# Performance work log

Hardware: AMD Instinct MI355X
Metric: run time of the kernel (lower is better)

## Reference

```python
import jax, jax.numpy as jnp
import numpy as np

K = 9        # kNN neighbors (ViG default kernel_size=9)
EPS = 1e-5   # BatchNorm eps


def _bn2d(x, gamma, beta):
    # training-mode BatchNorm2d over (B,H,W) per channel; x: [B,C,H,W]
    mean = jnp.mean(x, axis=(0, 2, 3), keepdims=True)
    var = jnp.var(x, axis=(0, 2, 3), keepdims=True)
    g = gamma.reshape(1, -1, 1, 1)
    b = beta.reshape(1, -1, 1, 1)
    return g * (x - mean) * jax.lax.rsqrt(var + EPS) + b


def setup_inputs() -> dict:
    key = jax.random.key(0)
    B, C, H, W = 8, 96, 56, 56
    oup = 192
    ks = jax.random.split(key, 8)
    sc = 0.05
    return {
        "x": jax.random.normal(ks[0], (B, C, H, W), dtype=jnp.float32),
        "W_fc1": jax.random.normal(ks[1], (C, C), dtype=jnp.float32) * sc,
        "b_fc1": jnp.zeros((C,), jnp.float32),
        "g_bn1": jnp.ones((C,), jnp.float32),
        "be_bn1": jnp.zeros((C,), jnp.float32),
        "W_edge": jax.random.normal(ks[2], (2 * C, 2 * C), dtype=jnp.float32) * sc,
        "b_edge": jnp.zeros((2 * C,), jnp.float32),
        "g_bne": jnp.ones((2 * C,), jnp.float32),
        "be_bne": jnp.zeros((2 * C,), jnp.float32),
        "W_fc2": jax.random.normal(ks[3], (2 * C, C), dtype=jnp.float32) * sc,
        "b_fc2": jnp.zeros((C,), jnp.float32),
        "g_bn2": jnp.ones((C,), jnp.float32),
        "be_bn2": jnp.zeros((C,), jnp.float32),
        "g_sabn": jnp.ones((C,), jnp.float32),
        "be_sabn": jnp.zeros((C,), jnp.float32),
        "W_dw": jax.random.normal(ks[4], (oup, C, 3, 3), dtype=jnp.float32) * sc,
        "b_dw": jnp.zeros((oup,), jnp.float32),
        "g_dwbn": jnp.ones((oup,), jnp.float32),
        "be_dwbn": jnp.zeros((oup,), jnp.float32),
    }


def reference(x, W_fc1, b_fc1, g_bn1, be_bn1, W_edge, b_edge, g_bne, be_bne,
              W_fc2, b_fc2, g_bn2, be_bn2, g_sabn, be_sabn,
              W_dw, b_dw, g_dwbn, be_dwbn):
    B, C, H, W = x.shape
    N = H * W
    shortcut = x

    # --- Grapher.fc1: 1x1 conv + BN ---
    y = jnp.einsum('bchw,cd->bdhw', x, W_fc1) + b_fc1[None, :, None, None]
    y = _bn2d(y, g_bn1, be_bn1)

    # --- dynamic kNN graph over flattened tokens ---
    ft = y.reshape(B, C, N).transpose(0, 2, 1)            # [B,N,C]
    sq = jnp.sum(ft * ft, axis=-1)                        # [B,N]
    dist = sq[:, :, None] - 2.0 * jnp.einsum('bnc,bmc->bnm', ft, ft) + sq[:, None, :]
    _, idx = jax.lax.top_k(-dist, K)                      # [B,N,K] nearest neighbors

    # --- EdgeConv: max_k act(BN(W [x_i, x_j - x_i])) ---
    x_j = jnp.take_along_axis(ft[:, :, None, :], idx[..., None], axis=1)  # [B,N,K,C]
    x_i = ft[:, :, None, :]                               # [B,N,1,C]
    e = jnp.concatenate([jnp.broadcast_to(x_i, x_j.shape), x_j - x_i], axis=-1)  # [B,N,K,2C]
    e = jnp.einsum('bnkc,cd->bnkd', e, W_edge) + b_edge
    m = jnp.mean(e, axis=(0, 1, 2))
    v = jnp.var(e, axis=(0, 1, 2))
    e = g_bne * (e - m) * jax.lax.rsqrt(v + EPS) + be_bne
    e = jax.nn.relu(e)
    g = jnp.max(e, axis=2)                                # [B,N,2C] max-aggregation

    # --- Grapher.fc2: 1x1 conv + BN, residual ---
    g = jnp.einsum('bnc,cd->bnd', g, W_fc2) + b_fc2       # [B,N,C]
    g = g.transpose(0, 2, 1).reshape(B, C, H, W)
    g = _bn2d(g, g_bn2, be_bn2)
    y = g + shortcut

    # --- SAEncoder: BN + ReLU ---
    y = jax.nn.relu(_bn2d(y, g_sabn, be_sabn))

    # --- convdw: 3x3 stride-2 conv + BN + ReLU ---
    y = jax.lax.conv_general_dilated(
        y, W_dw, window_strides=(2, 2), padding=((1, 1), (1, 1)),
        dimension_numbers=('NCHW', 'OIHW', 'NCHW')) + b_dw[None, :, None, None]
    y = jax.nn.relu(_bn2d(y, g_dwbn, be_dwbn))
    return y
```

## Files before the change

kernel.cpp:

```cpp
#include <hip/hip_runtime.h>
#include <math.h>

#define B_   8
#define C_   96
#define C2_  192
#define N_   3136
#define R_   25088
#define OUP_ 192
#define HO_  28
#define NO_  784
#define EPS_ 1e-5f
#define QS2  128
#define CAP3 64

typedef short bf16x8 __attribute__((ext_vector_type(8)));
typedef float f32x4  __attribute__((ext_vector_type(4)));

__device__ __forceinline__ int swz16(int i) { return (i & ~15) | ((i & 15) ^ ((i >> 4) & 7)); }

__global__ __launch_bounds__(512) void k_fc1_d(const float* __restrict__ x,
                                               const float* __restrict__ W1,
                                               const float* __restrict__ b1,
                                               double* __restrict__ yd) {
    __shared__ double Wl[96 * 48];
    int tid = threadIdx.x;
    int rl = tid & 255, h = tid >> 8;
    int dbase = blockIdx.y * 48;
    for (int q = tid; q < 96 * 48; q += 512) {
        int c = q / 48, dd = q % 48;
        Wl[c * 48 + dd] = (double)W1[c * 96 + dbase + dd];
    }
    __syncthreads();
    int r = blockIdx.x * 256 + rl;
    int b = r / N_;
    int n = r - b * N_;
    double acc[24];
#pragma unroll
    for (int i = 0; i < 24; i++) acc[i] = 0.0;
    const float* xp = x + (size_t)b * C_ * N_ + n;
    for (int c = 0; c < 96; ++c) {
        double xv = (double)xp[(size_t)c * N_];
        const double* w = &Wl[c * 48 + h * 24];
#pragma unroll
        for (int i = 0; i < 24; ++i) acc[i] += xv * w[i];
    }
    int d0 = dbase + h * 24;
#pragma unroll
    for (int i = 0; i < 24; i++) {
        int d = d0 + i;
        yd[((size_t)b * C_ + d) * N_ + n] = acc[i] + (double)b1[d];
    }
}

__global__ __launch_bounds__(256) void k_stats_chan_d(const double* __restrict__ src,
                                                      double* __restrict__ partial) {
    int c = blockIdx.x;
    int chunk = blockIdx.y;
    const int SPLIT = 16;
    double s = 0.0, ss = 0.0;
    for (int j = chunk * 256 + threadIdx.x; j < R_; j += SPLIT * 256) {
        int b = j / N_, n = j - b * N_;
        double v = src[((size_t)b * C_ + c) * N_ + n];
        s += v;
        ss += v * v;
    }
    __shared__ double red[8];
    for (int off = 32; off; off >>= 1) {
        s += __shfl_down(s, off, 64);
        ss += __shfl_down(ss, off, 64);
    }
    int lane = threadIdx.x & 63, w = threadIdx.x >> 6;
    if (lane == 0) { red[w * 2] = s; red[w * 2 + 1] = ss; }
    __syncthreads();
    if (threadIdx.x == 0) {
        s = red[0] + red[2] + red[4] + red[6];
        ss = red[1] + red[3] + red[5] + red[7];
        partial[(c * SPLIT + chunk) * 2] = s;
        partial[(c * SPLIT + chunk) * 2 + 1] = ss;
    }
}

__global__ void k_stats_reduce_d(const double* __restrict__ partial, double* __restrict__ stats) {
    int c = blockIdx.x * blockDim.x + threadIdx.x;
    if (c >= 96) return;
    double s = 0.0, ss = 0.0;
    for (int k = 0; k < 16; k++) {
        s += partial[(c * 16 + k) * 2];
        ss += partial[(c * 16 + k) * 2 + 1];
    }
    double m = s / (double)R_;
    double var = ss / (double)R_ - m * m;
    stats[c * 2] = m;
    stats[c * 2 + 1] = 1.0 / sqrt(var + 1e-5);
}

__global__ void k_stats_reduce(const float* __restrict__ partial, float* __restrict__ stats,
                               int Cn, int SPLIT, float invcount) {
    int c = blockIdx.x * blockDim.x + threadIdx.x;
    if (c >= Cn) return;
    float s = 0.f, ss = 0.f;
    for (int k = 0; k < SPLIT; k++) {
        s += partial[(c * SPLIT + k) * 2];
        ss += partial[(c * SPLIT + k) * 2 + 1];
    }
    float m = s * invcount;
    float var = ss * invcount - m * m;
    stats[c * 2] = m;
    stats[c * 2 + 1] = 1.0f / sqrtf(var + EPS_);
}

__global__ __launch_bounds__(256) void k_stats_reduce_g(const float* __restrict__ partial,
                                                        float* __restrict__ stats,
                                                        int Cn, int NB, float invcount) {
    int c = blockIdx.x;
    float s = 0.f, ss = 0.f;
    for (int k = threadIdx.x; k < NB; k += 256) {
        s  += partial[(size_t)k * 2 * Cn + c];
        ss += partial[(size_t)k * 2 * Cn + Cn + c];
    }
    __shared__ float red[8];
    for (int off = 32; off; off >>= 1) {
        s += __shfl_down(s, off, 64);
        ss += __shfl_down(ss, off, 64);
    }
    int lane = threadIdx.x & 63, w = threadIdx.x >> 6;
    if (lane == 0) { red[w * 2] = s; red[w * 2 + 1] = ss; }
    __syncthreads();
    if (threadIdx.x == 0) {
        s = red[0] + red[2] + red[4] + red[6];
        ss = red[1] + red[3] + red[5] + red[7];
        float m = s * invcount;
        float var = ss * invcount - m * m;
        stats[c * 2] = m;
        stats[c * 2 + 1] = 1.0f / sqrtf(var + EPS_);
    }
}

__global__ __launch_bounds__(256) void k_bn1_tr(const double* __restrict__ yd,
                                                const double* __restrict__ stats,
                                                const float* __restrict__ g,
                                                const float* __restrict__ be,
                                                float* __restrict__ ftc,
                                                double* __restrict__ ftp64,
                                                unsigned short* __restrict__ fspH,
                                                double* __restrict__ sq64,
                                                unsigned* __restrict__ poolCnt) {
    __shared__ double tile[64 * 97];
    __shared__ double dsq[64][4];
    int b = blockIdx.y;
    int n0 = blockIdx.x * 64;
    int tid = threadIdx.x;
    int n = tid & 63, w = tid >> 6;
    for (int k = 0; k < 24; ++k) {
        int c = k * 4 + w;
        size_t gi = ((size_t)b * C_ + c) * N_ + n0 + n;
        double m = stats[c * 2], rs = stats[c * 2 + 1];
        double v = (double)g[c] * (yd[gi] - m) * rs + (double)be[c];
        ftc[gi] = (float)v;
        tile[n * 97 + c] = v;
    }
    __syncthreads();
    int p = n, q = w;
    double vals[24];
    double s = 0.0;
    const double* lp = &tile[p * 97 + q * 24];
#pragma unroll
    for (int m2 = 0; m2 < 24; ++m2) { vals[m2] = lp[m2]; s += vals[m2] * vals[m2]; }
    dsq[p][q] = s;
    double* dst = ftp64 + ((size_t)b * N_ + n0 + p) * C_ + q * 24;
#pragma unroll
    for (int m2 = 0; m2 < 24; m2 += 2) *(double2*)&dst[m2] = make_double2(vals[m2], vals[m2 + 1]);
    unsigned* hdst = (unsigned*)(fspH + ((size_t)b * N_ + n0 + p) * QS2);
#pragma unroll
    for (int m2 = 0; m2 < 24; m2 += 2) {
        unsigned u0 = __float_as_uint((float)vals[m2]);
        unsigned u1 = __float_as_uint((float)vals[m2 + 1]);
        unsigned h0 = (u0 + 0x7fffu + ((u0 >> 16) & 1u)) >> 16;
        unsigned h1 = (u1 + 0x7fffu + ((u1 >> 16) & 1u)) >> 16;
        hdst[q * 12 + (m2 >> 1)] = h0 | (h1 << 16);
    }
    __syncthreads();
    if (tid < 64) {
        double tot = dsq[tid][0] + dsq[tid][1] + dsq[tid][2] + dsq[tid][3];
        sq64[(size_t)b * N_ + n0 + tid] = tot;
        poolCnt[(size_t)b * N_ + n0 + tid] = 0u;
        float t32 = (float)(-0.5 * tot);
        unsigned u0 = __float_as_uint(t32);
        unsigned h0 = (u0 + 0x7fffu + ((u0 >> 16) & 1u)) >> 16;
        float resid = t32 - __uint_as_float(h0 << 16);
        unsigned u1 = __float_as_uint(resid);
        unsigned h1 = (u1 + 0x7fffu + ((u1 >> 16) & 1u)) >> 16;
        unsigned* hd = (unsigned*)(fspH + ((size_t)b * N_ + n0 + tid) * QS2);
        hd[48] = h0 | (h1 << 16);
#pragma unroll
        for (int k2 = 49; k2 < 64; ++k2) hd[k2] = 0u;
    }
}

__global__ __launch_bounds__(256) void k_dist5(const unsigned short* __restrict__ fspH,
                                               unsigned short* __restrict__ poolC,
                                               unsigned* __restrict__ poolCnt) {
    __shared__ __align__(16) char lds[39680];
    float* cminF = (float*)(lds + 32768);
    float* t9fL  = (float*)(lds + 39168);
    int b = blockIdx.z, half = blockIdx.y;
    int q0 = blockIdx.x * 64;
    int tid = threadIdx.x, w = tid >> 6, l = tid & 63;
    int ch0 = half * 25, nch = half ? 24 : 25;
    int qg = b * N_ + q0 + w * 16 + (l & 15);

    {
        const uint4* src = (const uint4*)(fspH + ((size_t)b * N_ + q0) * QS2);
        uint4* dst = (uint4*)lds;
        for (int i = tid; i < 1024; i += 256) dst[swz16(i)] = src[i];
    }
    __syncthreads();
    bf16x8 Bq[4];
    {
        const unsigned short* Ql = (const unsigned short*)lds;
        int qr = w * 16 + (l & 15);
#pragma unroll
        for (int s = 0; s < 3; ++s) {
            int col = (s * 4 + (l >> 4)) ^ (qr & 7);
            Bq[s] = *(const bf16x8*)&Ql[qr * QS2 + col * 8];
        }
        bf16x8 z = {0, 0, 0, 0, 0, 0, 0, 0};
        if ((l >> 4) == 0) { z[0] = (short)0x3F80; z[1] = (short)0x3F80; }
        Bq[3] = z;
    }
    __syncthreads();

    {
        const uint4* src = (const uint4*)(fspH + ((size_t)b * N_ + ch0 * 64) * QS2);
        uint4* dst = (uint4*)lds;
        for (int i = tid; i < 1024; i += 256) dst[swz16(i)] = src[i];
    }
    __syncthreads();

    float thr2r = 1e30f;
    int cur = 0;
    int nct = 2 * nch;
    for (int t = 0; t < nct; ++t) {
        int chl = (t < nch) ? t : t - nch;
        int c0 = (ch0 + chl) * 64;
        bool pf = (t < nct - 1);
        uint4 st0, st1, st2, st3;
        if (pf) {
            int tn = t + 1;
            int nc = ch0 + ((tn < nch) ? tn : tn - nch);
            const uint4* src = (const uint4*)(fspH + ((size_t)b * N_ + nc * 64) * QS2);
            st0 = src[tid]; st1 = src[tid + 256]; st2 = src[tid + 512]; st3 = src[tid + 768];
        }
        const unsigned short* Bc = (const unsigned short*)(lds + cur * 16384);
        f32x4 acc[4];
#pragma unroll
        for (int ct = 0; ct < 4; ++ct) acc[ct] = (f32x4){0.f, 0.f, 0.f, 0.f};
#pragma unroll
        for (int s = 0; s < 4; ++s) {
#pragma unroll
            for (int ct = 0; ct < 4; ++ct) {
                int cr = ct * 16 + (l & 15);
                int col = (s * 4 + (l >> 4)) ^ (cr & 7);
                bf16x8 Ac = *(const bf16x8*)&Bc[cr * QS2 + col * 8];
                acc[ct] = __builtin_amdgcn_mfma_f32_16x16x32_bf16(Ac, Bq[s], acc[ct], 0, 0, 0);
            }
        }
        if (t < nch) {
            float mx = -1e30f;
#pragma unroll
            for (int ct = 0; ct < 4; ++ct)
#pragma unroll
                for (int j = 0; j < 4; ++j) mx = fmaxf(mx, acc[ct][j]);
            mx = fmaxf(mx, __shfl_xor(mx, 16, 64));
            mx = fmaxf(mx, __shfl_xor(mx, 32, 64));
            if (l < 16) cminF[chl * 64 + w * 16 + l] = -2.f * mx;
        } else {
#pragma unroll
            for (int ct = 0; ct < 4; ++ct)
#pragma unroll
                for (int j = 0; j < 4; ++j) {
                    if (acc[ct][j] >= thr2r) {
                        unsigned pos = atomicAdd(&poolCnt[qg], 1u);
                        if (pos < (unsigned)CAP3)
                            poolC[(size_t)qg * CAP3 + pos] = (unsigned short)(c0 + ct * 16 + (l >> 4) * 4 + j);
                    }
                }
        }
        if (t == nch - 1) {
            __syncthreads();
            if (tid < 64) {
                float top[9];
#pragma unroll
                for (int j = 0; j < 9; ++j) top[j] = 1e30f;
                for (int q = 0; q < nch; ++q) {
                    float v = cminF[q * 64 + tid];
                    if (v < top[8]) {
                        top[8] = v;
#pragma unroll
                        for (int j = 8; j >= 1; --j)
                            if (top[j] < top[j - 1]) { float tt = top[j]; top[j] = top[j - 1]; top[j - 1] = tt; }
                    }
                }
                float t9 = top[8] + fabsf(top[8]) * 0.008f + 0.75f;
                t9fL[tid] = -0.5f * t9;
            }
            __syncthreads();
            thr2r = t9fL[w * 16 + (l & 15)];
        }
        if (pf) {
            uint4* dst = (uint4*)(lds + (cur ^ 1) * 16384);
            dst[swz16(tid)] = st0;
            dst[swz16(tid + 256)] = st1;
            dst[swz16(tid + 512)] = st2;
            dst[swz16(tid + 768)] = st3;
        }
        __syncthreads();
        cur ^= 1;
    }
}

__global__ __launch_bounds__(256) void k_rerank_d(const unsigned short* __restrict__ poolC,
                                                  const unsigned* __restrict__ poolCnt,
                                                  const double* __restrict__ ftp64,
                                                  const double* __restrict__ sq64,
                                                  int* __restrict__ idx) {
    int tid = threadIdx.x;
    int wv = tid >> 6, l = tid & 63;
    int rr = blockIdx.x * 4 + wv;
    int b = rr / N_;
    int cnt = (int)poolCnt[rr];
    if (cnt > CAP3) cnt = CAP3;
    int e = l & 3;
    double qreg[24];
    {
        const double* qb = ftp64 + (size_t)rr * C_ + e * 24;
#pragma unroll
        for (int m = 0; m < 24; ++m) qreg[m] = qb[m];
    }
    double dv[4];
    int jv[4];
#pragma unroll
    for (int gG = 0; gG < 4; ++gG) { dv[gG] = 1e300; jv[gG] = 0x7fffffff; }
#pragma unroll
    for (int gG = 0; gG < 4; ++gG) {
        if (gG * 16 >= cnt) break;
        int ci = gG * 16 + (l >> 2);
        bool valid = ci < cnt;
        int j = valid ? (int)poolC[(size_t)rr * CAP3 + ci] : 0;
        const double* cb = ftp64 + ((size_t)b * N_ + j) * C_ + e * 24;
        double p = 0.0;
#pragma unroll
        for (int m = 0; m < 24; ++m) p += qreg[m] * cb[m];
        p += __shfl_xor(p, 1, 64);
        p += __shfl_xor(p, 2, 64);
        if (valid) {
            dv[gG] = sq64[(size_t)b * N_ + j] - 2.0 * p;
            jv[gG] = j;
        }
    }
#pragma unroll
    for (int r = 0; r < 9; ++r) {
        double dm = dv[0]; int jm = jv[0];
#pragma unroll
        for (int gG = 1; gG < 4; ++gG)
            if (dv[gG] < dm || (dv[gG] == dm && jv[gG] < jm)) { dm = dv[gG]; jm = jv[gG]; }
#pragma unroll
        for (int off = 1; off <= 32; off <<= 1) {
            double od = __shfl_xor(dm, off, 64);
            int oj = __shfl_xor(jm, off, 64);
            if (od < dm || (od == dm && oj < jm)) { dm = od; jm = oj; }
        }
        if (l == 0) idx[(size_t)rr * 9 + r] = jm;
#pragma unroll
        for (int gG = 0; gG < 4; ++gG)
            if (jv[gG] == jm) dv[gG] = 1e300;
    }
}

__global__ __launch_bounds__(512) void k_gemm_uv2(const float* __restrict__ ftc,
                                                  const float* __restrict__ We,
                                                  const float* __restrict__ beb,
                                                  float* __restrict__ u,
                                                  float* __restrict__ v) {
    __shared__ float Wl[2][96 * 48];
    int tid = threadIdx.x;
    int rl = tid & 255, h = tid >> 8;
    int dbase = blockIdx.y * 48;
    for (int q = tid; q < 96 * 48; q += 512) {
        int c = q / 48, dd = q % 48;
        float wb = We[(96 + c) * C2_ + dbase + dd];
        Wl[1][q] = wb;
        Wl[0][q] = We[c * C2_ + dbase + dd] - wb;
    }
    __syncthreads();
    int r = blockIdx.x * 256 + rl;
    int b = r / N_, n = r - b * N_;
    float a0[24], a1[24];
#pragma unroll
    for (int i = 0; i < 24; i++) { a0[i] = 0.f; a1[i] = 0.f; }
    const float* xp = ftc + (size_t)b * C_ * N_ + n;
    for (int c = 0; c < 96; ++c) {
        float xv = xp[(size_t)c * N_];
        const float4* w40 = (const float4*)&Wl[0][c * 48 + h * 24];
        const float4* w41 = (const float4*)&Wl[1][c * 48 + h * 24];
#pragma unroll
        for (int i = 0; i < 6; ++i) {
            float4 w0 = w40[i], w1 = w41[i];
            a0[i * 4 + 0] += xv * w0.x; a0[i * 4 + 1] += xv * w0.y;
            a0[i * 4 + 2] += xv * w0.z; a0[i * 4 + 3] += xv * w0.w;
            a1[i * 4 + 0] += xv * w1.x; a1[i * 4 + 1] += xv * w1.y;
            a1[i * 4 + 2] += xv * w1.z; a1[i * 4 + 3] += xv * w1.w;
        }
    }
    int d0 = dbase + h * 24;
    float* up = u + (size_t)r * C2_ + d0;
    float* vp = v + (size_t)r * C2_ + d0;
#pragma unroll
    for (int i = 0; i < 6; ++i) {
        float4 ou, ov;
        ou.x = a0[i * 4 + 0] + beb[d0 + i * 4 + 0];
        ou.y = a0[i * 4 + 1] + beb[d0 + i * 4 + 1];
        ou.z = a0[i * 4 + 2] + beb[d0 + i * 4 + 2];
        ou.w = a0[i * 4 + 3] + beb[d0 + i * 4 + 3];
        ov.x = a1[i * 4 + 0]; ov.y = a1[i * 4 + 1];
        ov.z = a1[i * 4 + 2]; ov.w = a1[i * 4 + 3];
        ((float4*)up)[i] = ou;
        ((float4*)vp)[i] = ov;
    }
}

__global__ __launch_bounds__(192) void k_bne_stats(const float* __restrict__ u,
                                                   const float* __restrict__ v,
                                                   const int* __restrict__ idx,
                                                   float* __restrict__ partial) {
    int d = threadIdx.x;
    int row0 = blockIdx.x * 32;
    int b = row0 / N_;
    float s = 0.f, ss = 0.f;
    for (int r = 0; r < 32; ++r) {
        int row = row0 + r;
        float ud = u[(size_t)row * C2_ + d];
        const int* ip = idx + (size_t)row * 9;
#pragma unroll
        for (int k = 0; k < 9; k++) {
            int j = ip[k];
            float e = ud + v[((size_t)b * N_ + j) * C2_ + d];
            s += e;
            ss += e * e;
        }
    }
    partial[(size_t)blockIdx.x * 384 + d] = s;
    partial[(size_t)blockIdx.x * 384 + 192 + d] = ss;
}

__global__ __launch_bounds__(192) void k_edge_fc2_st(const float* __restrict__ u,
                                                     const float* __restrict__ v,
                                                     const int* __restrict__ idx,
                                                     const float* __restrict__ statsE,
                                                     const float* __restrict__ ge,
                                                     const float* __restrict__ bee,
                                                     const float* __restrict__ W2,
                                                     const float* __restrict__ b2,
                                                     float* __restrict__ out2,
                                                     float* __restrict__ partialE) {
    __shared__ float gl[16][C2_];
    __shared__ float g2[C_][16];
    int tid = threadIdx.x;
    int row0 = blockIdx.x * 16;
    int b = row0 / N_;
    int n0 = row0 - b * N_;
    {
        int d = tid;
        float m = statsE[d * 2], rs = statsE[d * 2 + 1];
        float ga = ge[d], bb = bee[d];
        for (int r = 0; r < 16; ++r) {
            int row = row0 + r;
            float ud = u[(size_t)row * C2_ + d];
            const int* ip = idx + (size_t)row * 9;
            float gm = 0.f;
#pragma unroll
            for (int k = 0; k < 9; k++) {
                int j = ip[k];
                float e = ud + v[((size_t)b * N_ + j) * C2_ + d];
                float val = ga * (e - m) * rs + bb;
                gm = fmaxf(gm, val);
            }
            gl[r][d] = gm;
        }
    }
    __syncthreads();
    {
        int rr = tid / 24;
        int dq = tid % 24;
        for (int rep = 0; rep < 2; ++rep) {
            int r = rr + rep * 8;
            float4 acc = *(const float4*)&b2[dq * 4];
            for (int d = 0; d < C2_; ++d) {
                float gv = gl[r][d];
                float4 w = *(const float4*)&W2[d * C_ + dq * 4];
                acc.x += gv * w.x;
                acc.y += gv * w.y;
                acc.z += gv * w.z;
                acc.w += gv * w.w;
            }
            g2[dq * 4 + 0][r] = acc.x;
            g2[dq * 4 + 1][r] = acc.y;
            g2[dq * 4 + 2][r] = acc.z;
            g2[dq * 4 + 3][r] = acc.w;
        }
    }
    __syncthreads();
    for (int q = tid; q < 96 * 4; q += 192) {
        int dd = q / 4, part = q % 4;
        float4 val = *(const float4*)&g2[dd][part * 4];
        *(float4*)&out2[((size_t)b * C_ + dd) * N_ + n0 + part * 4] = val;
    }
    {
        int c = tid >> 1, h = tid & 1;
        float s = 0.f, ss = 0.f;
#pragma unroll
        for (int r = 0; r < 8; ++r) {
            float vv = g2[c][h * 8 + r];
            s += vv;
            ss += vv * vv;
        }
        s += __shfl_xor(s, 1, 64);
        ss += __shfl_xor(ss, 1, 64);
        if (h == 0) {
            partialE[(size_t)blockIdx.x * 192 + c] = s;
            partialE[(size_t)blockIdx.x * 192 + 96 + c] = ss;
        }
    }
}

__global__ __launch_bounds__(256) void k_bn2_add_st(const float* __restrict__ out2,
                                                    const float* __restrict__ x,
                                                    const float* __restrict__ stats,
                                                    const float* __restrict__ g,
                                                    const float* __restrict__ be,
                                                    float* __restrict__ t,
                                                    float* __restrict__ partial) {
    int c = blockIdx.x;
    int chunk = blockIdx.y;
    const int SPLIT = 16;
    float m = stats[c * 2], rs = stats[c * 2 + 1];
    float ga = g[c], bb = be[c];
    float s = 0.f, ss = 0.f;
    for (int j = chunk * 256 + threadIdx.x; j < R_; j += SPLIT * 256) {
        int b = j / N_, n = j - b * N_;
        size_t i = ((size_t)b * C_ + c) * N_ + n;
        float tv = ga * (out2[i] - m) * rs + bb + x[i];
        t[i] = tv;
        s += tv;
        ss += tv * tv;
    }
    __shared__ float red[8];
    for (int off = 32; off; off >>= 1) {
        s += __shfl_down(s, off, 64);
        ss += __shfl_down(ss, off, 64);
    }
    int lane = threadIdx.x & 63, w = threadIdx.x >> 6;
    if (lane == 0) { red[w * 2] = s; red[w * 2 + 1] = ss; }
    __syncthreads();
    if (threadIdx.x == 0) {
        s = red[0] + red[2] + red[4] + red[6];
        ss = red[1] + red[3] + red[5] + red[7];
        partial[(c * SPLIT + chunk) * 2] = s;
        partial[(c * SPLIT + chunk) * 2 + 1] = ss;
    }
}

__global__ __launch_bounds__(256) void k_conv8(const float* __restrict__ t,
                                               const float* __restrict__ statsS,
                                               const float* __restrict__ gS,
                                               const float* __restrict__ beS,
                                               const float* __restrict__ Wd,
                                               const float* __restrict__ bd,
                                               float* __restrict__ z,
                                               float* __restrict__ partialD) {
    __shared__ float Wl[96 * 9 * 8];
    __shared__ float scl[96], shf[96];
    __shared__ float redc[4][16];
    int b = blockIdx.z;
    int oc0 = blockIdx.y * 8;
    int p = blockIdx.x * 256 + threadIdx.x;
    for (int i = threadIdx.x; i < 96 * 9 * 8; i += 256) {
        int oc = i & 7, icq = i >> 3;
        Wl[i] = Wd[(size_t)(oc0 + oc) * 864 + icq];
    }
    if (threadIdx.x < 96) {
        int c = threadIdx.x;
        float m = statsS[c * 2], rs = statsS[c * 2 + 1], ga = gS[c];
        scl[c] = ga * rs;
        shf[c] = beS[c] - ga * m * rs;
    }
    __syncthreads();
    bool valid = p < NO_;
    int oh = valid ? p / HO_ : 0, ow = valid ? p % HO_ : 0;
    float acc[8];
#pragma unroll
    for (int i = 0; i < 8; i++) acc[i] = 0.f;
    int ih0 = oh * 2 - 1, iw0 = ow * 2 - 1;
    const float* tb = t + (size_t)b * C_ * N_;
    for (int ic = 0; ic < 96; ++ic) {
        const float* sp = tb + (size_t)ic * N_;
        float sc_ = scl[ic], sh_ = shf[ic];
        float in[9];
#pragma unroll
        for (int kh = 0; kh < 3; kh++) {
            int ih = ih0 + kh;
            bool okh = valid && ((unsigned)ih < 56u);
#pragma unroll
            for (int kw = 0; kw < 3; kw++) {
                int iw = iw0 + kw;
                bool ok = okh && ((unsigned)iw < 56u);
                float raw = ok ? sp[ih * 56 + iw] : 0.f;
                in[kh * 3 + kw] = ok ? fmaxf(sc_ * raw + sh_, 0.f) : 0.f;
            }
        }
#pragma unroll
        for (int q = 0; q < 9; q++) {
            float iv = in[q];
            const float4* w4 = (const float4*)&Wl[(ic * 9 + q) * 8];
#pragma unroll
            for (int j = 0; j < 2; j++) {
                float4 w = w4[j];
                acc[j * 4 + 0] += iv * w.x;
                acc[j * 4 + 1] += iv * w.y;
                acc[j * 4 + 2] += iv * w.z;
                acc[j * 4 + 3] += iv * w.w;
            }
        }
    }
    float s8[8];
#pragma unroll
    for (int i = 0; i < 8; i++) {
        float ov = acc[i] + bd[oc0 + i];
        if (valid) z[((size_t)b * OUP_ + oc0 + i) * NO_ + p] = ov;
        s8[i] = valid ? ov : 0.f;
    }
    int w = threadIdx.x >> 6;
#pragma unroll
    for (int i = 0; i < 8; ++i) {
        float s = s8[i], ss = s8[i] * s8[i];
        for (int off = 32; off; off >>= 1) {
            s += __shfl_down(s, off, 64);
            ss += __shfl_down(ss, off, 64);
        }
        if ((threadIdx.x & 63) == 0) { redc[w][i * 2] = s; redc[w][i * 2 + 1] = ss; }
    }
    __syncthreads();
    if (threadIdx.x < 16) {
        float v = redc[0][threadIdx.x] + redc[1][threadIdx.x] + redc[2][threadIdx.x] + redc[3][threadIdx.x];
        int blk = (b * 24 + blockIdx.y) * 4 + blockIdx.x;
        partialD[blk * 16 + threadIdx.x] = v;
    }
}

__global__ void k_stats_reduce_conv(const float* __restrict__ partialD, float* __restrict__ stats) {
    int c = threadIdx.x;
    if (c >= 192) return;
    int y = c >> 3, o = c & 7;
    float s = 0.f, ss = 0.f;
    for (int bb = 0; bb < 8; ++bb)
        for (int x2 = 0; x2 < 4; ++x2) {
            int blk = (bb * 24 + y) * 4 + x2;
            s += partialD[blk * 16 + o * 2];
            ss += partialD[blk * 16 + o * 2 + 1];
        }
    float m = s / 6272.f;
    float var = ss / 6272.f - m * m;
    stats[c * 2] = m;
    stats[c * 2 + 1] = 1.0f / sqrtf(var + EPS_);
}

__global__ __launch_bounds__(256) void k_out(const float* __restrict__ z,
                                             const float* __restrict__ stats,
                                             const float* __restrict__ g,
                                             const float* __restrict__ be,
                                             float* __restrict__ out) {
    int i = blockIdx.x * 256 + threadIdx.x;
    if (i >= B_ * OUP_ * NO_) return;
    int c = (i / NO_) % OUP_;
    out[i] = fmaxf(g[c] * (z[i] - stats[c * 2]) * stats[c * 2 + 1] + be[c], 0.f);
}

extern "C" void kernel_launch(void* const* d_in, const int* in_sizes, int n_in,
                              void* d_out, int out_size, void* d_ws, size_t ws_size,
                              hipStream_t stream) {
    const float* x     = (const float*)d_in[0];
    const float* W_fc1 = (const float*)d_in[1];
    const float* b_fc1 = (const float*)d_in[2];
    const float* g_bn1 = (const float*)d_in[3];
    const float* be_bn1= (const float*)d_in[4];
    const float* W_edge= (const float*)d_in[5];
    const float* b_edge= (const float*)d_in[6];
    const float* g_bne = (const float*)d_in[7];
    const float* be_bne= (const float*)d_in[8];
    const float* W_fc2 = (const float*)d_in[9];
    const float* b_fc2 = (const float*)d_in[10];
    const float* g_bn2 = (const float*)d_in[11];
    const float* be_bn2= (const float*)d_in[12];
    const float* g_sabn= (const float*)d_in[13];
    const float* be_sabn=(const float*)d_in[14];
    const float* W_dw  = (const float*)d_in[15];
    const float* b_dw  = (const float*)d_in[16];
    const float* g_dwbn= (const float*)d_in[17];
    const float* be_dwbn=(const float*)d_in[18];

    char* base = (char*)d_ws;
    float*  ftc   = (float*)(base + 0);
    double* ftp64 = (double*)(base + 9633792);
    float*  uu    = (float*)(base + 9633792);
    double* yd    = (double*)(base + 28901376);
    float*  vv    = (float*)(base + 28901376);
    unsigned short* fspH = (unsigned short*)(base + 48168960);
    float*  out2  = (float*)(base + 48168960);
    unsigned short* poolC = (unsigned short*)(base + 57802752);
    float*  tbuf  = (float*)(base + 57802752);
    double* sq64  = (double*)(base + 67436544);
    int*    idx   = (int*)(base + 67637248);
    unsigned* poolCnt = (unsigned*)(base + 68540416);
    float*  partial = (float*)(base + 68741120);
    double* partiald = (double*)(base + 68741120);
    double* stats1d = (double*)(base + 69945344);
    float*  statsE  = (float*)(base + 69946880);
    float*  stats2  = (float*)(base + 69948416);
    float*  statsS  = (float*)(base + 69949952);
    float*  statsD  = (float*)(base + 69951488);
    float*  zbuf  = (float*)(base + 69953024);

    k_fc1_d<<<dim3(98, 2), 512, 0, stream>>>(x, W_fc1, b_fc1, yd);
    k_stats_chan_d<<<dim3(96, 16), 256, 0, stream>>>(yd, partiald);
    k_stats_reduce_d<<<1, 256, 0, stream>>>(partiald, stats1d);
    k_bn1_tr<<<dim3(49, B_), 256, 0, stream>>>(yd, stats1d, g_bn1, be_bn1, ftc, ftp64, fspH, sq64, poolCnt);

    k_dist5<<<dim3(49, 2, B_), 256, 0, stream>>>(fspH, poolC, poolCnt);
    k_rerank_d<<<6272, 256, 0, stream>>>(poolC, poolCnt, ftp64, sq64, idx);

    k_gemm_uv2<<<dim3(98, 4), 512, 0, stream>>>(ftc, W_edge, b_edge, uu, vv);

    k_bne_stats<<<784, 192, 0, stream>>>(uu, vv, idx, partial);
    k_stats_reduce_g<<<192, 256, 0, stream>>>(partial, statsE, 192, 784, 1.0f / 225792.0f);
    k_edge_fc2_st<<<1568, 192, 0, stream>>>(uu, vv, idx, statsE, g_bne, be_bne, W_fc2, b_fc2, out2, partial);
    k_stats_reduce_g<<<96, 256, 0, stream>>>(partial, stats2, 96, 1568, 1.0f / (float)R_);

    k_bn2_add_st<<<dim3(96, 16), 256, 0, stream>>>(out2, x, stats2, g_bn2, be_bn2, tbuf, partial);
    k_stats_reduce<<<1, 256, 0, stream>>>(partial, statsS, 96, 16, 1.0f / (float)R_);

    k_conv8<<<dim3(4, 24, 8), 256, 0, stream>>>(tbuf, statsS, g_sabn, be_sabn, W_dw, b_dw, zbuf, partial);
    k_stats_reduce_conv<<<1, 192, 0, stream>>>(partial, statsD);
    k_out<<<4705, 256, 0, stream>>>(zbuf, statsD, g_dwbn, be_dwbn, (float*)d_out);
}
```

Before: 692.3 us.

## Scan full candidate range per block in kNN and widen conv to 16 channels

The distance kernel now lets each block scan all 49 candidate chunks instead of splitting them into two halves. Candidate pools and their counters live in LDS and are written out once at the end, which removes the global atomics and the counter reset in the BN kernel. Separately, the depthwise conv computes 16 output channels per block and reads a pre-transposed weight array from global memory instead of staging weights in LDS. The cost is fewer blocks for both the distance and conv kernels, which lowers parallelism, plus an extra transpose kernel and more LDS per distance block.

```diff
diff --git a/kernel.cpp b/kernel.cpp
--- a/kernel.cpp
+++ b/kernel.cpp
@@ -143,8 +143,7 @@
                                                 float* __restrict__ ftc,
                                                 double* __restrict__ ftp64,
                                                 unsigned short* __restrict__ fspH,
-                                                double* __restrict__ sq64,
-                                                unsigned* __restrict__ poolCnt) {
+                                                double* __restrict__ sq64) {
     __shared__ double tile[64 * 97];
     __shared__ double dsq[64][4];
     int b = blockIdx.y;
@@ -183,7 +182,6 @@
     if (tid < 64) {
         double tot = dsq[tid][0] + dsq[tid][1] + dsq[tid][2] + dsq[tid][3];
         sq64[(size_t)b * N_ + n0 + tid] = tot;
-        poolCnt[(size_t)b * N_ + n0 + tid] = 0u;
         float t32 = (float)(-0.5 * tot);
         unsigned u0 = __float_as_uint(t32);
         unsigned h0 = (u0 + 0x7fffu + ((u0 >> 16) & 1u)) >> 16;
@@ -197,17 +195,19 @@
     }
 }
 
-__global__ __launch_bounds__(256) void k_dist5(const unsigned short* __restrict__ fspH,
+__global__ __launch_bounds__(256) void k_dist6(const unsigned short* __restrict__ fspH,
                                                unsigned short* __restrict__ poolC,
                                                unsigned* __restrict__ poolCnt) {
-    __shared__ __align__(16) char lds[39680];
-    float* cminF = (float*)(lds + 32768);
-    float* t9fL  = (float*)(lds + 39168);
-    int b = blockIdx.z, half = blockIdx.y;
+    __shared__ __align__(16) char lds[54016];
+    float*          cminF = (float*)(lds + 32768);
+    unsigned short* poolL = (unsigned short*)(lds + 45312);
+    unsigned*       cntL  = (unsigned*)(lds + 53504);
+    float*          t9fL  = (float*)(lds + 53760);
+
+    int b = blockIdx.y;
     int q0 = blockIdx.x * 64;
-    int tid = threadIdx.x, w = tid >> 6, l = tid & 63;
-    int ch0 = half * 25, nch = half ? 24 : 25;
-    int qg = b * N_ + q0 + w * 16 + (l & 15);
+    int tid = threadIdx.x;
+    int w = tid >> 6, l = tid & 63;
 
     {
         const uint4* src = (const uint4*)(fspH + ((size_t)b * N_ + q0) * QS2);
@@ -231,7 +231,7 @@
     __syncthreads();
 
     {
-        const uint4* src = (const uint4*)(fspH + ((size_t)b * N_ + ch0 * 64) * QS2);
+        const uint4* src = (const uint4*)(fspH + (size_t)b * N_ * QS2);
         uint4* dst = (uint4*)lds;
         for (int i = tid; i < 1024; i += 256) dst[swz16(i)] = src[i];
     }
@@ -239,16 +239,14 @@
 
     float thr2r = 1e30f;
     int cur = 0;
-    int nct = 2 * nch;
-    for (int t = 0; t < nct; ++t) {
-        int chl = (t < nch) ? t : t - nch;
-        int c0 = (ch0 + chl) * 64;
-        bool pf = (t < nct - 1);
+    for (int t = 0; t < 98; ++t) {
+        int ch = (t < 49) ? t : t - 49;
+        int c0 = ch * 64;
+        bool pf = (t < 97);
         uint4 st0, st1, st2, st3;
         if (pf) {
-            int tn = t + 1;
-            int nc = ch0 + ((tn < nch) ? tn : tn - nch);
-            const uint4* src = (const uint4*)(fspH + ((size_t)b * N_ + nc * 64) * QS2);
+            int nch = (t + 1 < 49) ? (t + 1) : (t + 1 - 49);
+            const uint4* src = (const uint4*)(fspH + ((size_t)b * N_ + nch * 64) * QS2);
             st0 = src[tid]; st1 = src[tid + 256]; st2 = src[tid + 512]; st3 = src[tid + 768];
         }
         const unsigned short* Bc = (const unsigned short*)(lds + cur * 16384);
@@ -265,7 +263,7 @@
                 acc[ct] = __builtin_amdgcn_mfma_f32_16x16x32_bf16(Ac, Bq[s], acc[ct], 0, 0, 0);
             }
         }
-        if (t < nch) {
+        if (t < 49) {
             float mx = -1e30f;
 #pragma unroll
             for (int ct = 0; ct < 4; ++ct)
@@ -273,26 +271,27 @@
                 for (int j = 0; j < 4; ++j) mx = fmaxf(mx, acc[ct][j]);
             mx = fmaxf(mx, __shfl_xor(mx, 16, 64));
             mx = fmaxf(mx, __shfl_xor(mx, 32, 64));
-            if (l < 16) cminF[chl * 64 + w * 16 + l] = -2.f * mx;
+            if (l < 16) cminF[ch * 64 + w * 16 + l] = -2.f * mx;
         } else {
+            int qrow = w * 16 + (l & 15);
 #pragma unroll
             for (int ct = 0; ct < 4; ++ct)
 #pragma unroll
                 for (int j = 0; j < 4; ++j) {
                     if (acc[ct][j] >= thr2r) {
-                        unsigned pos = atomicAdd(&poolCnt[qg], 1u);
+                        unsigned pos = atomicAdd(&cntL[qrow], 1u);
                         if (pos < (unsigned)CAP3)
-                            poolC[(size_t)qg * CAP3 + pos] = (unsigned short)(c0 + ct * 16 + (l >> 4) * 4 + j);
+                            poolL[qrow * CAP3 + pos] = (unsigned short)(c0 + ct * 16 + (l >> 4) * 4 + j);
                     }
                 }
         }
-        if (t == nch - 1) {
+        if (t == 48) {
             __syncthreads();
             if (tid < 64) {
                 float top[9];
 #pragma unroll
                 for (int j = 0; j < 9; ++j) top[j] = 1e30f;
-                for (int q = 0; q < nch; ++q) {
+                for (int q = 0; q < 49; ++q) {
                     float v = cminF[q * 64 + tid];
                     if (v < top[8]) {
                         top[8] = v;
@@ -303,6 +302,7 @@
                 }
                 float t9 = top[8] + fabsf(top[8]) * 0.008f + 0.75f;
                 t9fL[tid] = -0.5f * t9;
+                cntL[tid] = 0u;
             }
             __syncthreads();
             thr2r = t9fL[w * 16 + (l & 15)];
@@ -316,6 +316,15 @@
         }
         __syncthreads();
         cur ^= 1;
+    }
+    if (tid < 64) {
+        unsigned c = cntL[tid];
+        poolCnt[(size_t)b * N_ + q0 + tid] = (c > (unsigned)CAP3) ? (unsigned)CAP3 : c;
+    }
+    {
+        unsigned* dst = (unsigned*)(poolC + ((size_t)b * N_ + q0) * CAP3);
+        const unsigned* src = (const unsigned*)poolL;
+        for (int i = tid; i < 64 * CAP3 / 2; i += 256) dst[i] = src[i];
     }
 }
 
@@ -570,41 +579,37 @@
     }
 }
 
-__global__ __launch_bounds__(256) void k_conv8(const float* __restrict__ t,
-                                               const float* __restrict__ statsS,
-                                               const float* __restrict__ gS,
-                                               const float* __restrict__ beS,
-                                               const float* __restrict__ Wd,
-                                               const float* __restrict__ bd,
-                                               float* __restrict__ z,
-                                               float* __restrict__ partialD) {
-    __shared__ float Wl[96 * 9 * 8];
-    __shared__ float scl[96], shf[96];
-    __shared__ float redc[4][16];
+__global__ __launch_bounds__(256) void k_wtr(const float* __restrict__ Wd, float* __restrict__ Wt) {
+    int i = blockIdx.x * 256 + threadIdx.x;
+    if (i >= 192 * 864) return;
+    int oc = i / 864, k = i % 864;
+    Wt[(size_t)k * 192 + oc] = Wd[i];
+}
+
+__global__ __launch_bounds__(256) void k_conv16n(const float* __restrict__ t,
+                                                 const float* __restrict__ statsS,
+                                                 const float* __restrict__ gS,
+                                                 const float* __restrict__ beS,
+                                                 const float* __restrict__ Wt,
+                                                 const float* __restrict__ bd,
+                                                 float* __restrict__ z,
+                                                 float* __restrict__ partialD) {
+    __shared__ float redc[4][32];
     int b = blockIdx.z;
-    int oc0 = blockIdx.y * 8;
+    int oc0 = blockIdx.y * 16;
     int p = blockIdx.x * 256 + threadIdx.x;
-    for (int i = threadIdx.x; i < 96 * 9 * 8; i += 256) {
-        int oc = i & 7, icq = i >> 3;
-        Wl[i] = Wd[(size_t)(oc0 + oc) * 864 + icq];
-    }
-    if (threadIdx.x < 96) {
-        int c = threadIdx.x;
-        float m = statsS[c * 2], rs = statsS[c * 2 + 1], ga = gS[c];
-        scl[c] = ga * rs;
-        shf[c] = beS[c] - ga * m * rs;
-    }
-    __syncthreads();
     bool valid = p < NO_;
     int oh = valid ? p / HO_ : 0, ow = valid ? p % HO_ : 0;
-    float acc[8];
-#pragma unroll
-    for (int i = 0; i < 8; i++) acc[i] = 0.f;
+    float acc[16];
+#pragma unroll
+    for (int i = 0; i < 16; i++) acc[i] = 0.f;
     int ih0 = oh * 2 - 1, iw0 = ow * 2 - 1;
     const float* tb = t + (size_t)b * C_ * N_;
     for (int ic = 0; ic < 96; ++ic) {
+        float m = statsS[ic * 2], rs = statsS[ic * 2 + 1], ga = gS[ic];
+        float sc_ = ga * rs;
+        float sh_ = beS[ic] - ga * m * rs;
         const float* sp = tb + (size_t)ic * N_;
-        float sc_ = scl[ic], sh_ = shf[ic];
         float in[9];
 #pragma unroll
         for (int kh = 0; kh < 3; kh++) {
@@ -618,12 +623,13 @@
                 in[kh * 3 + kw] = ok ? fmaxf(sc_ * raw + sh_, 0.f) : 0.f;
             }
         }
+        const float* wk = Wt + (size_t)(ic * 9) * 192 + oc0;
 #pragma unroll
         for (int q = 0; q < 9; q++) {
             float iv = in[q];
-            const float4* w4 = (const float4*)&Wl[(ic * 9 + q) * 8];
-#pragma unroll
-            for (int j = 0; j < 2; j++) {
+            const float4* w4 = (const float4*)&wk[q * 192];
+#pragma unroll
+            for (int j = 0; j < 4; j++) {
                 float4 w = w4[j];
                 acc[j * 4 + 0] += iv * w.x;
                 acc[j * 4 + 1] += iv * w.y;
@@ -632,16 +638,16 @@
             }
         }
     }
-    float s8[8];
-#pragma unroll
-    for (int i = 0; i < 8; i++) {
+    float s8[16];
+#pragma unroll
+    for (int i = 0; i < 16; i++) {
         float ov = acc[i] + bd[oc0 + i];
         if (valid) z[((size_t)b * OUP_ + oc0 + i) * NO_ + p] = ov;
         s8[i] = valid ? ov : 0.f;
     }
     int w = threadIdx.x >> 6;
 #pragma unroll
-    for (int i = 0; i < 8; ++i) {
+    for (int i = 0; i < 16; ++i) {
         float s = s8[i], ss = s8[i] * s8[i];
         for (int off = 32; off; off >>= 1) {
             s += __shfl_down(s, off, 64);
@@ -650,23 +656,23 @@
         if ((threadIdx.x & 63) == 0) { redc[w][i * 2] = s; redc[w][i * 2 + 1] = ss; }
     }
     __syncthreads();
-    if (threadIdx.x < 16) {
+    if (threadIdx.x < 32) {
         float v = redc[0][threadIdx.x] + redc[1][threadIdx.x] + redc[2][threadIdx.x] + redc[3][threadIdx.x];
-        int blk = (b * 24 + blockIdx.y) * 4 + blockIdx.x;
-        partialD[blk * 16 + threadIdx.x] = v;
+        int blk = (b * 12 + blockIdx.y) * 4 + blockIdx.x;
+        partialD[blk * 32 + threadIdx.x] = v;
     }
 }
 
 __global__ void k_stats_reduce_conv(const float* __restrict__ partialD, float* __restrict__ stats) {
     int c = threadIdx.x;
     if (c >= 192) return;
-    int y = c >> 3, o = c & 7;
+    int y = c >> 4, o = c & 15;
     float s = 0.f, ss = 0.f;
     for (int bb = 0; bb < 8; ++bb)
         for (int x2 = 0; x2 < 4; ++x2) {
-            int blk = (bb * 24 + y) * 4 + x2;
-            s += partialD[blk * 16 + o * 2];
-            ss += partialD[blk * 16 + o * 2 + 1];
+            int blk = (bb * 12 + y) * 4 + x2;
+            s += partialD[blk * 32 + o * 2];
+            ss += partialD[blk * 32 + o * 2 + 1];
         }
     float m = s / 6272.f;
     float var = ss / 6272.f - m * m;
@@ -729,13 +735,16 @@
     float*  statsS  = (float*)(base + 69949952);
     float*  statsD  = (float*)(base + 69951488);
     float*  zbuf  = (float*)(base + 69953024);
+    float*  Wt    = (float*)(base + 74769920);
+
+    k_wtr<<<648, 256, 0, stream>>>(W_dw, Wt);
 
     k_fc1_d<<<dim3(98, 2), 512, 0, stream>>>(x, W_fc1, b_fc1, yd);
     k_stats_chan_d<<<dim3(96, 16), 256, 0, stream>>>(yd, partiald);
     k_stats_reduce_d<<<1, 256, 0, stream>>>(partiald, stats1d);
-    k_bn1_tr<<<dim3(49, B_), 256, 0, stream>>>(yd, stats1d, g_bn1, be_bn1, ftc, ftp64, fspH, sq64, poolCnt);
-
-    k_dist5<<<dim3(49, 2, B_), 256, 0, stream>>>(fspH, poolC, poolCnt);
+    k_bn1_tr<<<dim3(49, B_), 256, 0, stream>>>(yd, stats1d, g_bn1, be_bn1, ftc, ftp64, fspH, sq64);
+
+    k_dist6<<<dim3(49, B_), 256, 0, stream>>>(fspH, poolC, poolCnt);
     k_rerank_d<<<6272, 256, 0, stream>>>(poolC, poolCnt, ftp64, sq64, idx);
 
     k_gemm_uv2<<<dim3(98, 4), 512, 0, stream>>>(ftc, W_edge, b_edge, uu, vv);
@@ -748,7 +757,7 @@
     k_bn2_add_st<<<dim3(96, 16), 256, 0, stream>>>(out2, x, stats2, g_bn2, be_bn2, tbuf, partial);
     k_stats_reduce<<<1, 256, 0, stream>>>(partial, statsS, 96, 16, 1.0f / (float)R_);
 
-    k_conv8<<<dim3(4, 24, 8), 256, 0, stream>>>(tbuf, statsS, g_sabn, be_sabn, W_dw, b_dw, zbuf, partial);
+    k_conv16n<<<dim3(4, 12, 8), 256, 0, stream>>>(tbuf, statsS, g_sabn, be_sabn, Wt, b_dw, zbuf, partial);
     k_stats_reduce_conv<<<1, 192, 0, stream>>>(partial, statsD);
     k_out<<<4705, 256, 0, stream>>>(zbuf, statsD, g_dwbn, be_dwbn, (float*)d_out);
 }
```

New measurement: 685.9 us. About the same (-0.9%).
